# Kernel optimization log

Hardware: AMD Instinct MI355X
Metric: run time of the kernel (lower is better)

## Reference

```python
import jax, jax.numpy as jnp
import numpy as np

BETA = 0.25
B, D, H, W = 32, 256, 32, 32
K = 1024


def setup_inputs() -> dict:
    key = jax.random.key(0)
    k1, k2 = jax.random.split(key)
    inputs = jax.random.normal(k1, (B, D, H, W), dtype=jnp.float32)
    # torch init: uniform(-1/K, 1/K)
    codebook = jax.random.uniform(k2, (K, D), dtype=jnp.float32,
                                  minval=-1.0 / K, maxval=1.0 / K)
    return {"inputs": inputs, "codebook": codebook}


def reference(inputs, codebook):
    b, d, h, w = inputs.shape
    # (B, C, H, W) -> (B*H*W, D)
    x = inputs.transpose(0, 2, 3, 1).reshape(b * h * w, d)
    # Squared Euclidean distances; argmin is identical to cdist argmin.
    x2 = jnp.sum(x * x, axis=1, keepdims=True)            # (N, 1)
    c2 = jnp.sum(codebook * codebook, axis=1)             # (K,)
    d2 = x2 - 2.0 * (x @ codebook.T) + c2[None, :]        # (N, K)
    idx = jnp.argmin(d2, axis=1)                          # (N,)
    q = codebook[idx].reshape(b, h, w, d).transpose(0, 3, 1, 2)  # (B, D, H, W)

    q_loss = jnp.mean((q - jax.lax.stop_gradient(inputs)) ** 2)
    e_loss = jnp.mean((jax.lax.stop_gradient(q) - inputs) ** 2)
    vq_loss = q_loss + BETA * e_loss

    # straight-through estimator
    quantized = inputs + jax.lax.stop_gradient(q - inputs)
    return quantized, q_loss, e_loss, vq_loss, idx.reshape(b, h, w)
```

## Files before the change

### kernel.cpp

```cpp
#include <hip/hip_runtime.h>
#include <cstdint>

typedef float floatx4 __attribute__((ext_vector_type(4)));
typedef _Float16 half8 __attribute__((ext_vector_type(8)));
typedef _Float16 half4v __attribute__((ext_vector_type(4)));

#define D_DIM 256
#define HW 1024
#define K_CODES 1024
#define NPIX 32768
#define NELEM 8388608

#define OFF_QLOSS 8388608
#define OFF_ELOSS 8388609
#define OFF_VQ    8388610
#define OFF_IDX   8388611

#define WS_IDX     0
#define WS_C2      131072
#define WS_CNT     135168
#define WS_PART    135232
#define WS_FLAGPX  137280
#define WS_FLAGTOP 170048
#define FLAG_CAP   8192


#define MARGIN 2.5e-4f

__device__ __forceinline__ float np_pairwise_sq_256(const float* __restrict__ a, int stride) {
    float half[2];
#pragma unroll
    for (int h = 0; h < 2; ++h) {
        const float* p = a + (size_t)(h * 128) * stride;
        float r[8];
#pragma unroll
        for (int j = 0; j < 8; ++j) { float t = p[(size_t)j * stride]; r[j] = __fmul_rn(t, t); }
        for (int i = 8; i < 128; i += 8)
#pragma unroll
            for (int j = 0; j < 8; ++j) {
                float t = p[(size_t)(i + j) * stride];
                r[j] = __fadd_rn(r[j], __fmul_rn(t, t));
            }
        half[h] = __fadd_rn(__fadd_rn(__fadd_rn(r[0], r[1]), __fadd_rn(r[2], r[3])),
                            __fadd_rn(__fadd_rn(r[4], r[5]), __fadd_rn(r[6], r[7])));
    }
    return __fadd_rn(half[0], half[1]);
}

__global__ __launch_bounds__(256) void prep_kernel(const float* __restrict__ cb,
                                                   _Float16* __restrict__ cbh,
                                                   float* __restrict__ c2,
                                                   int* __restrict__ cnt) {
    int b = blockIdx.x;
    if (b < 256) {
        int i = (b * 256 + threadIdx.x) * 4;
        floatx4 v = *(const floatx4*)(cb + i);
        half4v o;
#pragma unroll
        for (int j = 0; j < 4; ++j) o[j] = (_Float16)(v[j] * 1024.0f);
        *(half4v*)(cbh + i) = o;
    } else {
        if (b == 256 && threadIdx.x == 0) *cnt = 0;
        int k = (b - 256) * 256 + threadIdx.x;
        c2[k] = np_pairwise_sq_256(cb + (size_t)k * D_DIM, 1);
    }
}

__device__ __forceinline__ void ins4v(float v, int k, float* S, int* I) {
    if (v < S[3]) {
        S[3] = v; I[3] = k;
#pragma unroll
        for (int j = 3; j > 0; --j) {
            if (S[j] < S[j - 1]) {
                float ts = S[j]; S[j] = S[j - 1]; S[j - 1] = ts;
                int   ti = I[j]; I[j] = I[j - 1]; I[j - 1] = ti;
            }
        }
    }
}

__global__ __launch_bounds__(256, 2) void gemm_stream(
        const float* __restrict__ x, const _Float16* __restrict__ cbh,
        const float* __restrict__ c2, float* __restrict__ out_idx,
        int* __restrict__ idxbuf, int* __restrict__ cnt,
        int* __restrict__ flagPx, floatx4* __restrict__ flagTop) {
    __shared__ float scr[4][32 * 65];

    const int t = threadIdx.x;
    const int w = t >> 6;
    const int l = t & 63;
    const int l15 = l & 15;
    const int q = l >> 4;
    const int pxg = w >> 1;
    const int half = w & 1;
    const int px0 = blockIdx.x * 64;
    const int bimg = px0 >> 10;
    const int hwb = (px0 & 1023) + pxg * 32;
    const float* xb = x + (size_t)bimg * (D_DIM * HW);

    half8 A[2][8];
#pragma unroll
    for (int r = 0; r < 2; ++r) {
        float tmp[64];
#pragma unroll
        for (int s = 0; s < 8; ++s)
#pragma unroll
            for (int j = 0; j < 8; ++j)
                tmp[s * 8 + j] = xb[(size_t)(s * 32 + q * 8 + j) * HW + hwb + r * 16 + l15];
#pragma unroll
        for (int s = 0; s < 8; ++s) {
            half8 h;
#pragma unroll
            for (int j = 0; j < 8; ++j) h[j] = (_Float16)tmp[s * 8 + j];
            A[r][s] = h;
        }
    }

    const _Float16* cbase = cbh + (size_t)(half * 512 + l15) * D_DIM;
    half8 B[2][8];
#pragma unroll
    for (int s = 0; s < 8; ++s)
        B[0][s] = *(const half8*)(cbase + s * 32 + q * 16 / 2);
    float c2cur = c2[half * 512 + l15];

    float m1[2][4], m2[2][4]; int i1[2][4], i2[2][4];
#pragma unroll
    for (int r = 0; r < 2; ++r)
#pragma unroll
        for (int a = 0; a < 4; ++a) {
            m1[r][a] = INFINITY; m2[r][a] = INFINITY; i1[r][a] = 0; i2[r][a] = 0;
        }

#pragma unroll 4
    for (int ch = 0; ch < 32; ++ch) {
        const int cur = ch & 1, nxt = cur ^ 1;
        float c2nxt = 0.f;
        if (ch < 31) {
            const _Float16* nb = cbase + (size_t)(ch + 1) * 16 * D_DIM;
#pragma unroll
            for (int s = 0; s < 8; ++s)
                B[nxt][s] = *(const half8*)(nb + s * 32 + q * 8);
            c2nxt = c2[half * 512 + (ch + 1) * 16 + l15];
        }
        floatx4 ac[2][2];
#pragma unroll
        for (int r = 0; r < 2; ++r)
#pragma unroll
            for (int h = 0; h < 2; ++h) ac[r][h] = floatx4{0.f, 0.f, 0.f, 0.f};
#pragma unroll
        for (int s = 0; s < 4; ++s) {
            ac[0][0] = __builtin_amdgcn_mfma_f32_16x16x32_f16(A[0][s],     B[cur][s],     ac[0][0], 0, 0, 0);
            ac[1][0] = __builtin_amdgcn_mfma_f32_16x16x32_f16(A[1][s],     B[cur][s],     ac[1][0], 0, 0, 0);
            ac[0][1] = __builtin_amdgcn_mfma_f32_16x16x32_f16(A[0][s + 4], B[cur][s + 4], ac[0][1], 0, 0, 0);
            ac[1][1] = __builtin_amdgcn_mfma_f32_16x16x32_f16(A[1][s + 4], B[cur][s + 4], ac[1][1], 0, 0, 0);
        }
        const int code = half * 512 + ch * 16 + l15;
#pragma unroll
        for (int r = 0; r < 2; ++r)
#pragma unroll
            for (int a = 0; a < 4; ++a) {
                float dot = ac[r][0][a] + ac[r][1][a];
                float s = fmaf(-0.001953125f, dot, c2cur);
                if (s < m1[r][a]) { m2[r][a] = m1[r][a]; i2[r][a] = i1[r][a]; m1[r][a] = s; i1[r][a] = code; }
                else if (s < m2[r][a]) { m2[r][a] = s; i2[r][a] = code; }
            }
        c2cur = c2nxt;
    }

    const int part = half * 16 + l15;
#pragma unroll
    for (int r = 0; r < 2; ++r)
#pragma unroll
        for (int a = 0; a < 4; ++a) {
            int px = pxg * 32 + r * 16 + q * 4 + a;
            int o = part * 65 + px;
            scr[0][o] = m1[r][a];
            scr[1][o] = __int_as_float(i1[r][a]);
            scr[2][o] = m2[r][a];
            scr[3][o] = __int_as_float(i2[r][a]);
        }
    __syncthreads();
    if (t < 64) {
        float S[4] = {INFINITY, INFINITY, INFINITY, INFINITY};
        int   I[4] = {0x7fffffff, 0x7fffffff, 0x7fffffff, 0x7fffffff};
        for (int p = 0; p < 32; ++p) {
            int o = p * 65 + t;
            ins4v(scr[0][o], __float_as_int(scr[1][o]), S, I);
            ins4v(scr[2][o], __float_as_int(scr[3][o]), S, I);
        }
        int P = px0 + t;
        idxbuf[P] = I[0];
        out_idx[P] = (float)I[0];
        if (S[1] - S[0] <= MARGIN) {
            int pos = atomicAdd(cnt, 1);
            if (pos < FLAG_CAP) {
                flagPx[pos] = P;
                flagTop[2 * pos]     = floatx4{S[0], (float)I[0], S[1], (float)I[1]};
                flagTop[2 * pos + 1] = floatx4{S[2], (float)I[2], S[3], (float)I[3]};
            }
        }
    }
}

__global__ __launch_bounds__(256) void rescore_wave(
        const float* __restrict__ x, const float* __restrict__ cb,
        const float* __restrict__ c2, const int* __restrict__ cnt,
        const int* __restrict__ flagPx, const floatx4* __restrict__ flagTop,
        float* __restrict__ out_idx, int* __restrict__ idxbuf) {
    const int wglobal = blockIdx.x * 4 + (threadIdx.x >> 6);
    const int l = threadIdx.x & 63;
    int n = *cnt; if (n > FLAG_CAP) n = FLAG_CAP;
    for (int i = wglobal; i < n; i += 1024) {
        int P = flagPx[i];
        floatx4 ta = flagTop[2 * i], tb = flagTop[2 * i + 1];
        float s1 = ta[0];
        float cs[4] = {ta[0], ta[2], tb[0], tb[2]};
        int   ck[4] = {(int)ta[1], (int)ta[3], (int)tb[1], (int)tb[3]};
        int nc = 1;
        while (nc < 4 && cs[nc] - s1 <= MARGIN) ++nc;

        const float* xcol = x + (size_t)(P >> 10) * D_DIM * HW + (P & 1023);

        float rj = 0.f;
        if (l < 16) {
            int h = l >> 3, j = l & 7;
            const float* p = xcol + (size_t)(h * 128) * HW;
            float v0 = p[(size_t)j * HW];
            rj = __fmul_rn(v0, v0);
            for (int ii = 1; ii < 16; ++ii) {
                float v = p[(size_t)(ii * 8 + j) * HW];
                rj = __fadd_rn(rj, __fmul_rn(v, v));
            }
        }
        float r0 = __shfl(rj, 0), r1 = __shfl(rj, 1), r2 = __shfl(rj, 2), r3 = __shfl(rj, 3);
        float r4 = __shfl(rj, 4), r5 = __shfl(rj, 5), r6 = __shfl(rj, 6), r7 = __shfl(rj, 7);
        float h0 = __fadd_rn(__fadd_rn(__fadd_rn(r0, r1), __fadd_rn(r2, r3)),
                             __fadd_rn(__fadd_rn(r4, r5), __fadd_rn(r6, r7)));
        r0 = __shfl(rj, 8); r1 = __shfl(rj, 9); r2 = __shfl(rj, 10); r3 = __shfl(rj, 11);
        r4 = __shfl(rj, 12); r5 = __shfl(rj, 13); r6 = __shfl(rj, 14); r7 = __shfl(rj, 15);
        float h1 = __fadd_rn(__fadd_rn(__fadd_rn(r0, r1), __fadd_rn(r2, r3)),
                             __fadd_rn(__fadd_rn(r4, r5), __fadd_rn(r6, r7)));
        float x2 = __fadd_rn(h0, h1);

        float xv[4];
#pragma unroll
        for (int u = 0; u < 4; ++u) xv[u] = xcol[(size_t)(l + u * 64) * HW];
        double accd[4] = {0.0, 0.0, 0.0, 0.0};
        for (int jc = 0; jc < nc; ++jc) {
            const float* cr = cb + (size_t)ck[jc] * D_DIM;
            double a = 0.0;
#pragma unroll
            for (int u = 0; u < 4; ++u) a += (double)xv[u] * (double)cr[l + u * 64];
#pragma unroll
            for (int off = 32; off > 0; off >>= 1) a += __shfl_down(a, off);
            accd[jc] = a;
        }
        if (l == 0) {
            float bd = INFINITY; int bi = 0x7fffffff;
            for (int jc = 0; jc < nc; ++jc) {
                float mm = (float)accd[jc];
                float t1 = __fsub_rn(x2, __fmul_rn(2.0f, mm));
                float Dq = __fadd_rn(t1, c2[ck[jc]]);
                if (Dq < bd || (Dq == bd && ck[jc] < bi)) { bd = Dq; bi = ck[jc]; }
            }
            idxbuf[P] = bi;
            out_idx[P] = (float)bi;
        }
    }
}

__global__ __launch_bounds__(128) void quantize_loss_kernel(
        const float* __restrict__ x, const float* __restrict__ cb,
        const int* __restrict__ idxbuf, float* __restrict__ out_q,
        double* __restrict__ partials) {
    int P = blockIdx.x * 128 + threadIdx.x;
    int bimg = P >> 10, hw = P & 1023;
    const float* xb = x + (size_t)bimg * D_DIM * HW + hw;
    float* qb = out_q + (size_t)bimg * D_DIM * HW + hw;
    const floatx4* crow = (const floatx4*)(cb + (size_t)idxbuf[P] * D_DIM);
    float lsum = 0.f;
#pragma unroll 4
    for (int d4 = 0; d4 < D_DIM / 4; ++d4) {
        floatx4 qv = crow[d4];
#pragma unroll
        for (int j = 0; j < 4; ++j) {
            size_t off = (size_t)(d4 * 4 + j) * HW;
            float xv = xb[off];
            qb[off] = qv[j];
            float df = qv[j] - xv;
            lsum = fmaf(df, df, lsum);
        }
    }
    double ds = (double)lsum;
#pragma unroll
    for (int off = 32; off > 0; off >>= 1) ds += __shfl_down(ds, off);
    __shared__ double sred[2];
    if ((threadIdx.x & 63) == 0) sred[threadIdx.x >> 6] = ds;
    __syncthreads();
    if (threadIdx.x == 0) partials[blockIdx.x] = sred[0] + sred[1];
}

__global__ __launch_bounds__(64) void finalize_loss(const double* __restrict__ partials,
                                                    float* __restrict__ out) {
    double s = 0.0;
    for (int i = threadIdx.x; i < 256; i += 64) s += partials[i];
#pragma unroll
    for (int off = 32; off > 0; off >>= 1) s += __shfl_down(s, off);
    if (threadIdx.x == 0) {
        double m = s / (double)NELEM;
        out[OFF_QLOSS] = (float)m;
        out[OFF_ELOSS] = (float)m;
        out[OFF_VQ]    = (float)(1.25 * m);
    }
}

extern "C" void kernel_launch(void* const* d_in, const int* in_sizes, int n_in,
                              void* d_out, int out_size, void* d_ws, size_t ws_size,
                              hipStream_t stream) {
    const float* x  = (const float*)d_in[0];
    const float* cb = (const float*)d_in[1];
    float* out = (float*)d_out;
    char* ws = (char*)d_ws;

    int*     idxbuf  = (int*)(ws + WS_IDX);
    float*   c2      = (float*)(ws + WS_C2);
    int*     cnt     = (int*)(ws + WS_CNT);
    double*  partials= (double*)(ws + WS_PART);
    int*     flagPx  = (int*)(ws + WS_FLAGPX);
    floatx4* flagTop = (floatx4*)(ws + WS_FLAGTOP);

    _Float16* cb16 = (_Float16*)out;

    prep_kernel<<<260, 256, 0, stream>>>(cb, cb16, c2, cnt);
    gemm_stream<<<512, 256, 0, stream>>>(x, cb16, c2, out + OFF_IDX, idxbuf,
                                         cnt, flagPx, flagTop);
    rescore_wave<<<256, 256, 0, stream>>>(x, cb, c2, cnt, flagPx, flagTop,
                                          out + OFF_IDX, idxbuf);
    quantize_loss_kernel<<<NPIX / 128, 128, 0, stream>>>(x, cb, idxbuf, out, partials);
    finalize_loss<<<1, 64, 0, stream>>>(partials, out);
}
```

Before: 189.1 us.

## Pre-swizzle codebook for coalesced MFMA loads and pack score/index into uint keys

```diff
diff --git a/kernel.cpp b/kernel.cpp
--- a/kernel.cpp
+++ b/kernel.cpp
@@ -18,14 +18,15 @@
 
 #define WS_IDX     0
 #define WS_C2      131072
-#define WS_CNT     135168
-#define WS_PART    135232
-#define WS_FLAGPX  137280
-#define WS_FLAGTOP 170048
+#define WS_C2P     135168
+#define WS_CNT     139264
+#define WS_PART    139328
+#define WS_FLAGPX  143424
+#define WS_FLAGTOP 176192
+#define WS_CBS     438336
 #define FLAG_CAP   8192
 
-
-#define MARGIN 2.5e-4f
+#define MARGIN 5.0e-4f
 
 __device__ __forceinline__ float np_pairwise_sq_256(const float* __restrict__ a, int stride) {
     float half[2];
@@ -48,155 +49,148 @@
 }
 
 __global__ __launch_bounds__(256) void prep_kernel(const float* __restrict__ cb,
-                                                   _Float16* __restrict__ cbh,
+                                                   _Float16* __restrict__ cbs,
                                                    float* __restrict__ c2,
+                                                   float* __restrict__ c2p,
                                                    int* __restrict__ cnt) {
     int b = blockIdx.x;
     if (b < 256) {
-        int i = (b * 256 + threadIdx.x) * 4;
-        floatx4 v = *(const floatx4*)(cb + i);
-        half4v o;
-#pragma unroll
-        for (int j = 0; j < 4; ++j) o[j] = (_Float16)(v[j] * 1024.0f);
-        *(half4v*)(cbh + i) = o;
+        int idx = b * 256 + threadIdx.x;
+        int c = idx >> 6;
+        int d = (idx & 63) * 4;
+        int s = d >> 5, q = (d >> 3) & 3, j0 = d & 7;
+        int quarter = c >> 8, ch = (c >> 4) & 15, l15 = c & 15;
+        int lane = q * 16 + l15;
+        size_t o = ((((size_t)(quarter * 16 + ch) * 8 + s) * 64 + lane) * 8 + j0);
+        floatx4 v = *(const floatx4*)(cb + (size_t)c * D_DIM + d);
+        half4v h;
+#pragma unroll
+        for (int j = 0; j < 4; ++j) h[j] = (_Float16)(v[j] * 1024.0f);
+        *(half4v*)(cbs + o) = h;
     } else {
         if (b == 256 && threadIdx.x == 0) *cnt = 0;
         int k = (b - 256) * 256 + threadIdx.x;
-        c2[k] = np_pairwise_sq_256(cb + (size_t)k * D_DIM, 1);
-    }
-}
-
-__device__ __forceinline__ void ins4v(float v, int k, float* S, int* I) {
+        float v = np_pairwise_sq_256(cb + (size_t)k * D_DIM, 1);
+        c2[k] = v;
+        c2p[k] = __fadd_rn(v, 1.0f);
+    }
+}
+
+__device__ __forceinline__ void ins4p(unsigned v, unsigned* S) {
     if (v < S[3]) {
-        S[3] = v; I[3] = k;
-#pragma unroll
-        for (int j = 3; j > 0; --j) {
-            if (S[j] < S[j - 1]) {
-                float ts = S[j]; S[j] = S[j - 1]; S[j - 1] = ts;
-                int   ti = I[j]; I[j] = I[j - 1]; I[j - 1] = ti;
-            }
-        }
-    }
-}
-
-__global__ __launch_bounds__(256, 2) void gemm_stream(
-        const float* __restrict__ x, const _Float16* __restrict__ cbh,
-        const float* __restrict__ c2, float* __restrict__ out_idx,
+        S[3] = v;
+#pragma unroll
+        for (int j = 3; j > 0; --j)
+            if (S[j] < S[j - 1]) { unsigned tmp = S[j]; S[j] = S[j - 1]; S[j - 1] = tmp; }
+    }
+}
+
+__global__ __launch_bounds__(256, 3) void gemm_swz(
+        const float* __restrict__ x, const _Float16* __restrict__ cbs,
+        const float* __restrict__ c2p, float* __restrict__ out_idx,
         int* __restrict__ idxbuf, int* __restrict__ cnt,
         int* __restrict__ flagPx, floatx4* __restrict__ flagTop) {
-    __shared__ float scr[4][32 * 65];
+    __shared__ uint2 scr[32][65];
 
     const int t = threadIdx.x;
     const int w = t >> 6;
     const int l = t & 63;
     const int l15 = l & 15;
     const int q = l >> 4;
-    const int pxg = w >> 1;
-    const int half = w & 1;
-    const int px0 = blockIdx.x * 64;
+    const int px0 = blockIdx.x * 32;
     const int bimg = px0 >> 10;
-    const int hwb = (px0 & 1023) + pxg * 32;
-    const float* xb = x + (size_t)bimg * (D_DIM * HW);
+    const int hwb = px0 & 1023;
+    const float* xb = x + (size_t)bimg * (D_DIM * HW) + hwb;
 
     half8 A[2][8];
 #pragma unroll
-    for (int r = 0; r < 2; ++r) {
-        float tmp[64];
-#pragma unroll
-        for (int s = 0; s < 8; ++s)
+    for (int r = 0; r < 2; ++r)
+#pragma unroll
+        for (int s = 0; s < 8; ++s) {
+            float tmp[8];
 #pragma unroll
             for (int j = 0; j < 8; ++j)
-                tmp[s * 8 + j] = xb[(size_t)(s * 32 + q * 8 + j) * HW + hwb + r * 16 + l15];
+                tmp[j] = xb[(size_t)(s * 32 + q * 8 + j) * HW + r * 16 + l15];
+            half8 h;
+#pragma unroll
+            for (int j = 0; j < 8; ++j) h[j] = (_Float16)tmp[j];
+            A[r][s] = h;
+        }
+
+    const _Float16* base = cbs + (size_t)w * 65536;
+    half8 B[2][8];
+#pragma unroll
+    for (int s = 0; s < 8; ++s)
+        B[0][s] = *(const half8*)(base + (size_t)s * 512 + l * 8);
+    float c2c = c2p[w * 256 + l15];
+
+    unsigned m1[2][4], m2[2][4];
+#pragma unroll
+    for (int r = 0; r < 2; ++r)
+#pragma unroll
+        for (int a = 0; a < 4; ++a) { m1[r][a] = 0xFFFFFFFFu; m2[r][a] = 0xFFFFFFFFu; }
+
+#pragma unroll 2
+    for (int ch = 0; ch < 16; ++ch) {
+        const int cur = ch & 1, nxt = cur ^ 1;
+        float c2n = 0.f;
+        if (ch < 15) {
+            const _Float16* nb = base + (size_t)(ch + 1) * 4096;
+#pragma unroll
+            for (int s = 0; s < 8; ++s)
+                B[nxt][s] = *(const half8*)(nb + (size_t)s * 512 + l * 8);
+            c2n = c2p[w * 256 + (ch + 1) * 16 + l15];
+        }
+        floatx4 acc[2];
+        acc[0] = floatx4{0.f, 0.f, 0.f, 0.f};
+        acc[1] = floatx4{0.f, 0.f, 0.f, 0.f};
 #pragma unroll
         for (int s = 0; s < 8; ++s) {
-            half8 h;
-#pragma unroll
-            for (int j = 0; j < 8; ++j) h[j] = (_Float16)tmp[s * 8 + j];
-            A[r][s] = h;
-        }
-    }
-
-    const _Float16* cbase = cbh + (size_t)(half * 512 + l15) * D_DIM;
-    half8 B[2][8];
-#pragma unroll
-    for (int s = 0; s < 8; ++s)
-        B[0][s] = *(const half8*)(cbase + s * 32 + q * 16 / 2);
-    float c2cur = c2[half * 512 + l15];
-
-    float m1[2][4], m2[2][4]; int i1[2][4], i2[2][4];
+            acc[0] = __builtin_amdgcn_mfma_f32_16x16x32_f16(A[0][s], B[cur][s], acc[0], 0, 0, 0);
+            acc[1] = __builtin_amdgcn_mfma_f32_16x16x32_f16(A[1][s], B[cur][s], acc[1], 0, 0, 0);
+        }
+        const unsigned code = (unsigned)(w * 256 + ch * 16 + l15);
+#pragma unroll
+        for (int r = 0; r < 2; ++r)
+#pragma unroll
+            for (int a = 0; a < 4; ++a) {
+                float sb = fmaf(-0.001953125f, acc[r][a], c2c);
+                unsigned p = (__float_as_uint(sb) & 0xFFFFFC00u) | code;
+                m2[r][a] = min(m2[r][a], max(m1[r][a], p));
+                m1[r][a] = min(m1[r][a], p);
+            }
+        c2c = c2n;
+    }
+
 #pragma unroll
     for (int r = 0; r < 2; ++r)
 #pragma unroll
         for (int a = 0; a < 4; ++a) {
-            m1[r][a] = INFINITY; m2[r][a] = INFINITY; i1[r][a] = 0; i2[r][a] = 0;
-        }
-
-#pragma unroll 4
-    for (int ch = 0; ch < 32; ++ch) {
-        const int cur = ch & 1, nxt = cur ^ 1;
-        float c2nxt = 0.f;
-        if (ch < 31) {
-            const _Float16* nb = cbase + (size_t)(ch + 1) * 16 * D_DIM;
-#pragma unroll
-            for (int s = 0; s < 8; ++s)
-                B[nxt][s] = *(const half8*)(nb + s * 32 + q * 8);
-            c2nxt = c2[half * 512 + (ch + 1) * 16 + l15];
-        }
-        floatx4 ac[2][2];
-#pragma unroll
-        for (int r = 0; r < 2; ++r)
-#pragma unroll
-            for (int h = 0; h < 2; ++h) ac[r][h] = floatx4{0.f, 0.f, 0.f, 0.f};
-#pragma unroll
-        for (int s = 0; s < 4; ++s) {
-            ac[0][0] = __builtin_amdgcn_mfma_f32_16x16x32_f16(A[0][s],     B[cur][s],     ac[0][0], 0, 0, 0);
-            ac[1][0] = __builtin_amdgcn_mfma_f32_16x16x32_f16(A[1][s],     B[cur][s],     ac[1][0], 0, 0, 0);
-            ac[0][1] = __builtin_amdgcn_mfma_f32_16x16x32_f16(A[0][s + 4], B[cur][s + 4], ac[0][1], 0, 0, 0);
-            ac[1][1] = __builtin_amdgcn_mfma_f32_16x16x32_f16(A[1][s + 4], B[cur][s + 4], ac[1][1], 0, 0, 0);
-        }
-        const int code = half * 512 + ch * 16 + l15;
-#pragma unroll
-        for (int r = 0; r < 2; ++r)
-#pragma unroll
-            for (int a = 0; a < 4; ++a) {
-                float dot = ac[r][0][a] + ac[r][1][a];
-                float s = fmaf(-0.001953125f, dot, c2cur);
-                if (s < m1[r][a]) { m2[r][a] = m1[r][a]; i2[r][a] = i1[r][a]; m1[r][a] = s; i1[r][a] = code; }
-                else if (s < m2[r][a]) { m2[r][a] = s; i2[r][a] = code; }
-            }
-        c2cur = c2nxt;
-    }
-
-    const int part = half * 16 + l15;
-#pragma unroll
-    for (int r = 0; r < 2; ++r)
-#pragma unroll
-        for (int a = 0; a < 4; ++a) {
-            int px = pxg * 32 + r * 16 + q * 4 + a;
-            int o = part * 65 + px;
-            scr[0][o] = m1[r][a];
-            scr[1][o] = __int_as_float(i1[r][a]);
-            scr[2][o] = m2[r][a];
-            scr[3][o] = __int_as_float(i2[r][a]);
+            int px = r * 16 + q * 4 + a;
+            scr[px][w * 16 + l15] = uint2{m1[r][a], m2[r][a]};
         }
     __syncthreads();
-    if (t < 64) {
-        float S[4] = {INFINITY, INFINITY, INFINITY, INFINITY};
-        int   I[4] = {0x7fffffff, 0x7fffffff, 0x7fffffff, 0x7fffffff};
-        for (int p = 0; p < 32; ++p) {
-            int o = p * 65 + t;
-            ins4v(scr[0][o], __float_as_int(scr[1][o]), S, I);
-            ins4v(scr[2][o], __float_as_int(scr[3][o]), S, I);
+    if (t < 32) {
+        unsigned S[4] = {0xFFFFFFFFu, 0xFFFFFFFFu, 0xFFFFFFFFu, 0xFFFFFFFFu};
+        for (int p = 0; p < 64; ++p) {
+            uint2 e = scr[t][p];
+            ins4p(e.x, S);
+            ins4p(e.y, S);
         }
         int P = px0 + t;
-        idxbuf[P] = I[0];
-        out_idx[P] = (float)I[0];
-        if (S[1] - S[0] <= MARGIN) {
+        int best = (int)(S[0] & 1023u);
+        idxbuf[P] = best;
+        out_idx[P] = (float)best;
+        float cs0 = __uint_as_float(S[0] & 0xFFFFFC00u);
+        float cs1 = __uint_as_float(S[1] & 0xFFFFFC00u);
+        if (cs1 - cs0 <= MARGIN) {
             int pos = atomicAdd(cnt, 1);
             if (pos < FLAG_CAP) {
+                float cs2 = __uint_as_float(S[2] & 0xFFFFFC00u);
+                float cs3 = __uint_as_float(S[3] & 0xFFFFFC00u);
                 flagPx[pos] = P;
-                flagTop[2 * pos]     = floatx4{S[0], (float)I[0], S[1], (float)I[1]};
-                flagTop[2 * pos + 1] = floatx4{S[2], (float)I[2], S[3], (float)I[3]};
+                flagTop[2 * pos]     = floatx4{cs0, (float)(S[0] & 1023u), cs1, (float)(S[1] & 1023u)};
+                flagTop[2 * pos + 1] = floatx4{cs2, (float)(S[2] & 1023u), cs3, (float)(S[3] & 1023u)};
             }
         }
     }
@@ -269,41 +263,45 @@
     }
 }
 
-__global__ __launch_bounds__(128) void quantize_loss_kernel(
+__global__ __launch_bounds__(256) void quantize_loss_kernel(
         const float* __restrict__ x, const float* __restrict__ cb,
         const int* __restrict__ idxbuf, float* __restrict__ out_q,
         double* __restrict__ partials) {
-    int P = blockIdx.x * 128 + threadIdx.x;
-    int bimg = P >> 10, hw = P & 1023;
+    const int t = threadIdx.x;
+    const int pxl = t & 63;
+    const int dg = t >> 6;
+    const int P = blockIdx.x * 64 + pxl;
+    const int bimg = P >> 10, hw = P & 1023;
     const float* xb = x + (size_t)bimg * D_DIM * HW + hw;
     float* qb = out_q + (size_t)bimg * D_DIM * HW + hw;
-    const floatx4* crow = (const floatx4*)(cb + (size_t)idxbuf[P] * D_DIM);
+    const floatx4* crow = (const floatx4*)(cb + (size_t)idxbuf[P] * D_DIM) + dg * 16;
     float lsum = 0.f;
 #pragma unroll 4
-    for (int d4 = 0; d4 < D_DIM / 4; ++d4) {
-        floatx4 qv = crow[d4];
+    for (int i = 0; i < 16; ++i) {
+        floatx4 cv = crow[i];
+        int dbase = dg * 64 + i * 4;
 #pragma unroll
         for (int j = 0; j < 4; ++j) {
-            size_t off = (size_t)(d4 * 4 + j) * HW;
+            size_t off = (size_t)(dbase + j) * HW;
             float xv = xb[off];
-            qb[off] = qv[j];
-            float df = qv[j] - xv;
+            qb[off] = cv[j];
+            float df = cv[j] - xv;
             lsum = fmaf(df, df, lsum);
         }
     }
     double ds = (double)lsum;
 #pragma unroll
     for (int off = 32; off > 0; off >>= 1) ds += __shfl_down(ds, off);
-    __shared__ double sred[2];
-    if ((threadIdx.x & 63) == 0) sred[threadIdx.x >> 6] = ds;
+    __shared__ double sred[4];
+    if ((t & 63) == 0) sred[t >> 6] = ds;
     __syncthreads();
-    if (threadIdx.x == 0) partials[blockIdx.x] = sred[0] + sred[1];
+    if (t == 0) partials[blockIdx.x] = sred[0] + sred[1] + sred[2] + sred[3];
 }
 
 __global__ __launch_bounds__(64) void finalize_loss(const double* __restrict__ partials,
                                                     float* __restrict__ out) {
     double s = 0.0;
-    for (int i = threadIdx.x; i < 256; i += 64) s += partials[i];
+    for (int i = threadIdx.x; i < 512; i += 64) s += partials[i];
 #pragma unroll
     for (int off = 32; off > 0; off >>= 1) s += __shfl_down(s, off);
     if (threadIdx.x == 0) {
@@ -322,20 +320,20 @@
     float* out = (float*)d_out;
     char* ws = (char*)d_ws;
 
-    int*     idxbuf  = (int*)(ws + WS_IDX);
-    float*   c2      = (float*)(ws + WS_C2);
-    int*     cnt     = (int*)(ws + WS_CNT);
-    double*  partials= (double*)(ws + WS_PART);
-    int*     flagPx  = (int*)(ws + WS_FLAGPX);
-    floatx4* flagTop = (floatx4*)(ws + WS_FLAGTOP);
-
-    _Float16* cb16 = (_Float16*)out;
-
-    prep_kernel<<<260, 256, 0, stream>>>(cb, cb16, c2, cnt);
-    gemm_stream<<<512, 256, 0, stream>>>(x, cb16, c2, out + OFF_IDX, idxbuf,
-                                         cnt, flagPx, flagTop);
+    int*      idxbuf  = (int*)(ws + WS_IDX);
+    float*    c2      = (float*)(ws + WS_C2);
+    float*    c2p     = (float*)(ws + WS_C2P);
+    int*      cnt     = (int*)(ws + WS_CNT);
+    double*   partials= (double*)(ws + WS_PART);
+    int*      flagPx  = (int*)(ws + WS_FLAGPX);
+    floatx4*  flagTop = (floatx4*)(ws + WS_FLAGTOP);
+    _Float16* cbs     = (_Float16*)(ws + WS_CBS);
+
+    prep_kernel<<<260, 256, 0, stream>>>(cb, cbs, c2, c2p, cnt);
+    gemm_swz<<<NPIX / 32, 256, 0, stream>>>(x, cbs, c2p, out + OFF_IDX, idxbuf,
+                                            cnt, flagPx, flagTop);
     rescore_wave<<<256, 256, 0, stream>>>(x, cb, c2, cnt, flagPx, flagTop,
                                           out + OFF_IDX, idxbuf);
-    quantize_loss_kernel<<<NPIX / 128, 128, 0, stream>>>(x, cb, idxbuf, out, partials);
+    quantize_loss_kernel<<<NPIX / 64, 256, 0, stream>>>(x, cb, idxbuf, out, partials);
     finalize_loss<<<1, 64, 0, stream>>>(partials, out);
 }
```

Result: slower. 309.0 us (+63.4%).

## Pre-swizzle fp16 codebook into MFMA lane order and widen quantize kernel parallelism

Applied to the files above, without the earlier changes.

```diff
diff --git a/kernel.cpp b/kernel.cpp
--- a/kernel.cpp
+++ b/kernel.cpp
@@ -20,10 +20,10 @@
 #define WS_C2      131072
 #define WS_CNT     135168
 #define WS_PART    135232
-#define WS_FLAGPX  137280
-#define WS_FLAGTOP 170048
+#define WS_FLAGPX  143424
+#define WS_FLAGTOP 176192
+#define WS_CBS     438336
 #define FLAG_CAP   8192
-
 
 #define MARGIN 2.5e-4f
 
@@ -48,17 +48,23 @@
 }
 
 __global__ __launch_bounds__(256) void prep_kernel(const float* __restrict__ cb,
-                                                   _Float16* __restrict__ cbh,
+                                                   _Float16* __restrict__ cbs,
                                                    float* __restrict__ c2,
                                                    int* __restrict__ cnt) {
     int b = blockIdx.x;
     if (b < 256) {
-        int i = (b * 256 + threadIdx.x) * 4;
-        floatx4 v = *(const floatx4*)(cb + i);
-        half4v o;
-#pragma unroll
-        for (int j = 0; j < 4; ++j) o[j] = (_Float16)(v[j] * 1024.0f);
-        *(half4v*)(cbh + i) = o;
+        int idx = b * 256 + threadIdx.x;
+        int c = idx >> 6;
+        int d = (idx & 63) * 4;
+        int s = d >> 5, q = (d >> 3) & 3, j0 = d & 7;
+        int half = c >> 9, ch = (c >> 4) & 31, l15 = c & 15;
+        int lane = q * 16 + l15;
+        size_t o = ((((size_t)(half * 32 + ch) * 8 + s) * 64 + lane) * 8 + j0);
+        floatx4 v = *(const floatx4*)(cb + (size_t)c * D_DIM + d);
+        half4v h;
+#pragma unroll
+        for (int j = 0; j < 4; ++j) h[j] = (_Float16)(v[j] * 1024.0f);
+        *(half4v*)(cbs + o) = h;
     } else {
         if (b == 256 && threadIdx.x == 0) *cnt = 0;
         int k = (b - 256) * 256 + threadIdx.x;
@@ -79,8 +85,8 @@
     }
 }
 
-__global__ __launch_bounds__(256, 2) void gemm_stream(
-        const float* __restrict__ x, const _Float16* __restrict__ cbh,
+__global__ __launch_bounds__(256, 2) void gemm_swz(
+        const float* __restrict__ x, const _Float16* __restrict__ cbs,
         const float* __restrict__ c2, float* __restrict__ out_idx,
         int* __restrict__ idxbuf, int* __restrict__ cnt,
         int* __restrict__ flagPx, floatx4* __restrict__ flagTop) {
@@ -116,11 +122,11 @@
         }
     }
 
-    const _Float16* cbase = cbh + (size_t)(half * 512 + l15) * D_DIM;
+    const _Float16* base = cbs + (size_t)half * 131072;
     half8 B[2][8];
 #pragma unroll
     for (int s = 0; s < 8; ++s)
-        B[0][s] = *(const half8*)(cbase + s * 32 + q * 16 / 2);
+        B[0][s] = *(const half8*)(base + (size_t)s * 512 + l * 8);
     float c2cur = c2[half * 512 + l15];
 
     float m1[2][4], m2[2][4]; int i1[2][4], i2[2][4];
@@ -134,13 +140,13 @@
 #pragma unroll 4
     for (int ch = 0; ch < 32; ++ch) {
         const int cur = ch & 1, nxt = cur ^ 1;
-        float c2nxt = 0.f;
+        float c2n = 0.f;
         if (ch < 31) {
-            const _Float16* nb = cbase + (size_t)(ch + 1) * 16 * D_DIM;
+            const _Float16* nb = base + (size_t)(ch + 1) * 4096;
 #pragma unroll
             for (int s = 0; s < 8; ++s)
-                B[nxt][s] = *(const half8*)(nb + s * 32 + q * 8);
-            c2nxt = c2[half * 512 + (ch + 1) * 16 + l15];
+                B[nxt][s] = *(const half8*)(nb + (size_t)s * 512 + l * 8);
+            c2n = c2[half * 512 + (ch + 1) * 16 + l15];
         }
         floatx4 ac[2][2];
 #pragma unroll
@@ -164,7 +170,7 @@
                 if (s < m1[r][a]) { m2[r][a] = m1[r][a]; i2[r][a] = i1[r][a]; m1[r][a] = s; i1[r][a] = code; }
                 else if (s < m2[r][a]) { m2[r][a] = s; i2[r][a] = code; }
             }
-        c2cur = c2nxt;
+        c2cur = c2n;
     }
 
     const int part = half * 16 + l15;
@@ -269,41 +275,45 @@
     }
 }
 
-__global__ __launch_bounds__(128) void quantize_loss_kernel(
+__global__ __launch_bounds__(256) void quantize_loss_kernel(
         const float* __restrict__ x, const float* __restrict__ cb,
         const int* __restrict__ idxbuf, float* __restrict__ out_q,
         double* __restrict__ partials) {
-    int P = blockIdx.x * 128 + threadIdx.x;
-    int bimg = P >> 10, hw = P & 1023;
+    const int t = threadIdx.x;
+    const int pxl = t & 31;
+    const int dg = t >> 5;
+    const int P = blockIdx.x * 32 + pxl;
+    const int bimg = P >> 10, hw = P & 1023;
     const float* xb = x + (size_t)bimg * D_DIM * HW + hw;
     float* qb = out_q + (size_t)bimg * D_DIM * HW + hw;
-    const floatx4* crow = (const floatx4*)(cb + (size_t)idxbuf[P] * D_DIM);
+    const floatx4* crow = (const floatx4*)(cb + (size_t)idxbuf[P] * D_DIM) + dg * 8;
     float lsum = 0.f;
-#pragma unroll 4
-    for (int d4 = 0; d4 < D_DIM / 4; ++d4) {
-        floatx4 qv = crow[d4];
+#pragma unroll
+    for (int i = 0; i < 8; ++i) {
+        floatx4 cv = crow[i];
+        int dbase = dg * 32 + i * 4;
 #pragma unroll
         for (int j = 0; j < 4; ++j) {
-            size_t off = (size_t)(d4 * 4 + j) * HW;
+            size_t off = (size_t)(dbase + j) * HW;
             float xv = xb[off];
-            qb[off] = qv[j];
-            float df = qv[j] - xv;
+            qb[off] = cv[j];
+            float df = cv[j] - xv;
             lsum = fmaf(df, df, lsum);
         }
     }
     double ds = (double)lsum;
 #pragma unroll
     for (int off = 32; off > 0; off >>= 1) ds += __shfl_down(ds, off);
-    __shared__ double sred[2];
-    if ((threadIdx.x & 63) == 0) sred[threadIdx.x >> 6] = ds;
+    __shared__ double sred[4];
+    if ((t & 63) == 0) sred[t >> 6] = ds;
     __syncthreads();
-    if (threadIdx.x == 0) partials[blockIdx.x] = sred[0] + sred[1];
+    if (t == 0) partials[blockIdx.x] = sred[0] + sred[1] + sred[2] + sred[3];
 }
 
 __global__ __launch_bounds__(64) void finalize_loss(const double* __restrict__ partials,
                                                     float* __restrict__ out) {
     double s = 0.0;
-    for (int i = threadIdx.x; i < 256; i += 64) s += partials[i];
+    for (int i = threadIdx.x; i < 1024; i += 64) s += partials[i];
 #pragma unroll
     for (int off = 32; off > 0; off >>= 1) s += __shfl_down(s, off);
     if (threadIdx.x == 0) {
@@ -322,20 +332,19 @@
     float* out = (float*)d_out;
     char* ws = (char*)d_ws;
 
-    int*     idxbuf  = (int*)(ws + WS_IDX);
-    float*   c2      = (float*)(ws + WS_C2);
-    int*     cnt     = (int*)(ws + WS_CNT);
-    double*  partials= (double*)(ws + WS_PART);
-    int*     flagPx  = (int*)(ws + WS_FLAGPX);
-    floatx4* flagTop = (floatx4*)(ws + WS_FLAGTOP);
-
-    _Float16* cb16 = (_Float16*)out;
-
-    prep_kernel<<<260, 256, 0, stream>>>(cb, cb16, c2, cnt);
-    gemm_stream<<<512, 256, 0, stream>>>(x, cb16, c2, out + OFF_IDX, idxbuf,
-                                         cnt, flagPx, flagTop);
+    int*      idxbuf  = (int*)(ws + WS_IDX);
+    float*    c2      = (float*)(ws + WS_C2);
+    int*      cnt     = (int*)(ws + WS_CNT);
+    double*   partials= (double*)(ws + WS_PART);
+    int*      flagPx  = (int*)(ws + WS_FLAGPX);
+    floatx4*  flagTop = (floatx4*)(ws + WS_FLAGTOP);
+    _Float16* cbs     = (_Float16*)(ws + WS_CBS);
+
+    prep_kernel<<<260, 256, 0, stream>>>(cb, cbs, c2, cnt);
+    gemm_swz<<<NPIX / 64, 256, 0, stream>>>(x, cbs, c2, out + OFF_IDX, idxbuf,
+                                            cnt, flagPx, flagTop);
     rescore_wave<<<256, 256, 0, stream>>>(x, cb, c2, cnt, flagPx, flagTop,
                                           out + OFF_IDX, idxbuf);
-    quantize_loss_kernel<<<NPIX / 128, 128, 0, stream>>>(x, cb, idxbuf, out, partials);
+    quantize_loss_kernel<<<NPIX / 32, 256, 0, stream>>>(x, cb, idxbuf, out, partials);
     finalize_loss<<<1, 64, 0, stream>>>(partials, out);
 }
```

New measurement: 152.9 us. 19.2% less time.
